# Kernel tuning notes

Hardware: AMD Instinct MI355X
Metric: run time of the kernel (lower is better)

Reference implementation:

```python
import jax, jax.numpy as jnp
import numpy as np

HIDDEN = 1024
N_HEADS = 16
HEAD = HIDDEN // N_HEADS
BATCH = 8
SEQ = 1024


def setup_inputs() -> dict:
    key = jax.random.key(0)
    ks = jax.random.split(key, 9)
    s = 0.02
    return {
        "x": jax.random.normal(ks[0], (BATCH, SEQ, HIDDEN), dtype=jnp.float32),
        "wq": jax.random.normal(ks[1], (HIDDEN, HIDDEN), dtype=jnp.float32) * s,
        "bq": jnp.zeros((HIDDEN,), dtype=jnp.float32),
        "wk": jax.random.normal(ks[2], (HIDDEN, HIDDEN), dtype=jnp.float32) * s,
        "bk": jnp.zeros((HIDDEN,), dtype=jnp.float32),
        "wv": jax.random.normal(ks[3], (HIDDEN, HIDDEN), dtype=jnp.float32) * s,
        "bv": jnp.zeros((HIDDEN,), dtype=jnp.float32),
        "wo": jax.random.normal(ks[4], (HIDDEN, HIDDEN), dtype=jnp.float32) * s,
        "bo": jnp.zeros((HIDDEN,), dtype=jnp.float32),
    }


def _split_heads(t):
    # [b, s, hidden] -> [b, head, s, head_size]
    b, s, _ = t.shape
    return t.reshape(b, s, N_HEADS, HEAD).transpose(0, 2, 1, 3)


def reference(x, wq, bq, wk, bk, wv, bv, wo, bo):
    # Linear layers (torch nn.Linear: y = x @ W.T + b); here weights stored as [in, out]
    q = _split_heads(x @ wq + bq)
    k = _split_heads(x @ wk + bk)
    v = _split_heads(x @ wv + bv)
    # NOTE: original scales by 1/sqrt(hidden_size), not 1/sqrt(head_size)
    scores = jnp.einsum("bhqd,bhkd->bhqk", q, k) / jnp.sqrt(jnp.float32(HIDDEN))
    attn = jax.nn.softmax(scores, axis=-1)
    combined = jnp.einsum("bhqk,bhkd->bhqd", attn, v)
    merged = combined.transpose(0, 2, 1, 3).reshape(x.shape[0], x.shape[1], HIDDEN)
    return merged @ wo + bo
```

## Files before the change

kernel.cpp:

```cpp
#include <hip/hip_runtime.h>
#include <hip/hip_bf16.h>

#define HIDDEN 1024
#define NHEADS 16
#define HEADD  64
#define BATCH  8
#define SEQ    1024
#define MROWS  (BATCH*SEQ)

typedef __bf16 bf16x8 __attribute__((ext_vector_type(8)));
typedef float  floatx4 __attribute__((ext_vector_type(4)));
typedef unsigned short ushort8_t __attribute__((ext_vector_type(8)));
typedef _Float16 f16x4 __attribute__((ext_vector_type(4)));
typedef _Float16 f16x2 __attribute__((ext_vector_type(2)));
typedef const __attribute__((address_space(1))) unsigned int* gas_u32p;
typedef __attribute__((address_space(3))) unsigned int* las_u32p;

__device__ __forceinline__ unsigned short f2bf(float f) {
  __hip_bfloat16 h = __float2bfloat16(f);
  return __builtin_bit_cast(unsigned short, h);
}

__device__ __forceinline__ bf16x8 ld_bf8(const unsigned short* p) {
  ushort8_t u = *(const ushort8_t*)p;
  return __builtin_bit_cast(bf16x8, u);
}

__device__ __forceinline__ f16x2 pk_f16(float a, float b) {
  return __builtin_bit_cast(f16x2, __builtin_amdgcn_cvt_pkrtz(a, b));
}

__device__ __forceinline__ void gload_lds16(const void* g, void* l) {
  __builtin_amdgcn_global_load_lds((gas_u32p)g, (las_u32p)l, 16, 0, 0);
}

__global__ __launch_bounds__(256) void cast_x_kernel(const float* __restrict__ in,
                                                     unsigned short* __restrict__ out) {
  int i = blockIdx.x * 256 + threadIdx.x;
  float4 v = ((const float4*)in)[i];
  ushort4 o = make_ushort4(f2bf(v.x), f2bf(v.y), f2bf(v.z), f2bf(v.w));
  ((ushort4*)out)[i] = o;
}

__global__ __launch_bounds__(256) void transpose_cast_w_kernel(
    const float* __restrict__ w0, const float* __restrict__ w1,
    const float* __restrict__ w2, const float* __restrict__ w3,
    unsigned short* __restrict__ o0, unsigned short* __restrict__ o1,
    unsigned short* __restrict__ o2, unsigned short* __restrict__ o3) {
  __shared__ __align__(16) unsigned short tile[64 * 68];
  const float* src = (blockIdx.z == 0) ? w0 : (blockIdx.z == 1) ? w1 : (blockIdx.z == 2) ? w2 : w3;
  unsigned short* dst = (blockIdx.z == 0) ? o0 : (blockIdx.z == 1) ? o1 : (blockIdx.z == 2) ? o2 : o3;
  const int k0 = blockIdx.x * 64, n0 = blockIdx.y * 64;
  const int tid = threadIdx.x;
#pragma unroll
  for (int it = 0; it < 4; ++it) {
    int c = tid + 256 * it;
    int row = c >> 4, f4 = c & 15;
    float4 v = *(const float4*)(src + (size_t)(k0 + row) * HIDDEN + n0 + 4 * f4);
    ushort4 u = make_ushort4(f2bf(v.x), f2bf(v.y), f2bf(v.z), f2bf(v.w));
    *(ushort4*)(&tile[row * 68 + 4 * f4]) = u;
  }
  __syncthreads();
#pragma unroll
  for (int it = 0; it < 2; ++it) {
    int c = tid + 256 * it;
    int nrow = c >> 3, kc = (c & 7) * 8;
    ushort8_t u;
#pragma unroll
    for (int j = 0; j < 8; ++j) u[j] = tile[(kc + j) * 68 + nrow];
    *(ushort8_t*)(dst + (size_t)(n0 + nrow) * HIDDEN + k0 + kc) = u;
  }
}

#define LDSA(buf, ks) ((buf) * 49152 + (ks) * 8192)
#define LDSB(buf, ks) ((buf) * 49152 + 16384 + (ks) * 16384)

#define BAR __builtin_amdgcn_s_barrier()
#define WLG do { asm volatile("s_waitcnt lgkmcnt(0)" ::: "memory"); \
                 __builtin_amdgcn_sched_barrier(0); } while (0)
#define WVM(n) asm volatile("s_waitcnt vmcnt(" #n ")" ::: "memory")

#define RDP(buf, ks) do {                                                          \
    _Pragma("unroll") for (int m_ = 0; m_ < 4; ++m_)                               \
      af[m_] = *(const bf16x8*)(ldsb + LDSA(buf, ks) +                             \
                                (wm * 64 + 16 * m_ + lr) * 64 + colx);             \
    _Pragma("unroll") for (int n_ = 0; n_ < 4; ++n_)                               \
      bc[n_] = *(const bf16x8*)(ldsb + LDSB(buf, ks) +                             \
                                (wn * 64 + 16 * n_ + lr) * 64 + colx);             \
  } while (0)

#define MM do {                                                                    \
    __builtin_amdgcn_s_setprio(1);                                                 \
    _Pragma("unroll") for (int m_ = 0; m_ < 4; ++m_)                               \
      _Pragma("unroll") for (int n_ = 0; n_ < 4; ++n_)                             \
        acc[m_][n_] = __builtin_amdgcn_mfma_f32_16x16x32_bf16(                     \
            af[m_], bc[n_], acc[m_][n_], 0, 0, 0);                                 \
    __builtin_amdgcn_s_setprio(0);                                                 \
  } while (0)

#define STG(buf, ks, kt) do {                                                      \
    int go_ = (kt) * 128 + (ks) * 64;                                              \
    gload_lds16(aS + go_,  ldsb + LDSA(buf, ks) + tid * 16);                       \
    gload_lds16(bS0 + go_, ldsb + LDSB(buf, ks) + tid * 16);                       \
    gload_lds16(bS1 + go_, ldsb + LDSB(buf, ks) + 8192 + tid * 16);                \
  } while (0)

template <int OUT>
__device__ __forceinline__ void gemm256_body(
    const unsigned short* __restrict__ A,
    const unsigned short* __restrict__ Bt,
    const float* __restrict__ bias,
    char* __restrict__ C, int ldC, float scale,
    char* ldsb) {
  const int tid = threadIdx.x;
  const int lane = tid & 63;
  const int wid = tid >> 6;
  const int wm = wid >> 2, wn = wid & 3;
  const int lr = lane & 15, q = lane >> 4;
  const int colx = (16 * q) ^ (((lr >> 3) & 1) << 5);

  const char *aS, *bS0, *bS1;
  {
    int linA = tid * 16;
    int lgA = linA ^ (((linA >> 9) & 1) << 5);
    aS = (const char*)A + (lgA >> 6) * 2048 + (lgA & 63);
    int linB0 = tid * 16, linB1 = 8192 + tid * 16;
    int lgB0 = linB0 ^ (((linB0 >> 9) & 1) << 5);
    int lgB1 = linB1 ^ (((linB1 >> 9) & 1) << 5);
    bS0 = (const char*)Bt + (lgB0 >> 6) * 2048 + (lgB0 & 63);
    bS1 = (const char*)Bt + (lgB1 >> 6) * 2048 + (lgB1 & 63);
  }

  floatx4 acc[4][4] = {};
  bf16x8 af[4], bc[4];

  STG(0, 0, 0); STG(0, 1, 0); STG(1, 0, 1);
  WVM(6);
  BAR;

  for (int i = 0; i < 7; ++i) {
    const int t1 = 2 * i + 1;
    RDP(0, 0); STG(1, 1, t1);     BAR; WVM(6); WLG; MM; BAR;
    RDP(0, 1); STG(0, 0, t1 + 1); BAR; WVM(6); WLG; MM; BAR;
    RDP(1, 0); STG(0, 1, t1 + 1); BAR; WVM(6); WLG; MM; BAR;
    RDP(1, 1); STG(1, 0, t1 + 2); BAR; WVM(6); WLG; MM; BAR;
  }
  RDP(0, 0); STG(1, 1, 15); BAR; WVM(6); WLG; MM; BAR;
  RDP(0, 1);                BAR; WVM(3); WLG; MM; BAR;
  RDP(1, 0);                BAR; WVM(0); WLG; MM; BAR;
  RDP(1, 1);                BAR;         WLG; MM;

  float cb[4];
  if constexpr (OUT != 2) {
#pragma unroll
    for (int n_ = 0; n_ < 4; ++n_) cb[n_] = bias[wn * 64 + 16 * n_ + lr];
  }
#pragma unroll
  for (int m_ = 0; m_ < 4; ++m_) {
    int row = wm * 64 + 16 * m_ + q * 4;
    float rb[4];
    if constexpr (OUT == 2) {
      float4 t = *(const float4*)&bias[row];
      rb[0] = t.x; rb[1] = t.y; rb[2] = t.z; rb[3] = t.w;
    }
#pragma unroll
    for (int n_ = 0; n_ < 4; ++n_) {
      int col = wn * 64 + 16 * n_ + lr;
#pragma unroll
      for (int r = 0; r < 4; ++r) {
        float v = (acc[m_][n_][r] + (OUT == 2 ? rb[r] : cb[n_])) * scale;
        int idx = (row + r) * ldC + col;
        if constexpr (OUT == 1)      ((unsigned short*)C)[idx] = f2bf(v);
        else if constexpr (OUT == 2) ((_Float16*)C)[idx] = (_Float16)v;
        else                         ((float*)C)[idx] = v;
      }
    }
  }
}

__global__ __launch_bounds__(512, 2) void gemm_qkv256_kernel(
    const unsigned short* __restrict__ xb,
    const unsigned short* __restrict__ wqkt,
    const unsigned short* __restrict__ wvt,
    const float* __restrict__ bq, const float* __restrict__ bk, const float* __restrict__ bv,
    unsigned short* __restrict__ Qb, unsigned short* __restrict__ Kb,
    _Float16* __restrict__ Vtout, float qscale) {
  __shared__ __align__(16) char lds[2 * 49152];
  const int bid = blockIdx.x;
  const int x = bid & 7;
  const int j = bid >> 3;
  if (j < 64) {
    int mt = x * 8 + (j & 7);
    int nq = j >> 3;
    int m0 = mt * 128, n0 = nq * 256;
    bool isQ = n0 < HIDDEN;
    int nc = isQ ? n0 : n0 - HIDDEN;
    unsigned short* C = (isQ ? Qb : Kb) + (size_t)m0 * HIDDEN + nc;
    gemm256_body<1>(xb + (size_t)m0 * HIDDEN, wqkt + (size_t)n0 * HIDDEN,
                    (isQ ? bq : bk) + nc, (char*)C, HIDDEN, isQ ? qscale : 1.0f, lds);
  } else {
    int j2 = j - 64;
    int m0 = x * 128;
    int n0 = j2 * 256;
    gemm256_body<2>(wvt + (size_t)m0 * HIDDEN, xb + (size_t)n0 * HIDDEN, bv + m0,
                    (char*)(Vtout + (size_t)m0 * MROWS + n0), MROWS, 1.0f, lds);
  }
}

__global__ __launch_bounds__(512, 2) void gemm_out256_kernel(
    const unsigned short* __restrict__ Mg, const unsigned short* __restrict__ wot,
    const float* __restrict__ bo, float* __restrict__ out) {
  __shared__ __align__(16) char lds[2 * 49152];
  const int bid = blockIdx.x;
  const int x = bid & 7;
  const int j = bid >> 3;
  int mt = x * 8 + (j & 7);
  int nt = j >> 3;
  int m0 = mt * 128, n0 = nt * 256;
  gemm256_body<0>(Mg + (size_t)m0 * HIDDEN, wot + (size_t)n0 * HIDDEN, bo + n0,
                  (char*)(out + (size_t)m0 * HIDDEN + n0), HIDDEN, 1.0f, lds);
}

#undef RDP
#undef MM
#undef STG
#undef BAR
#undef WLG
#undef WVM
#undef LDSA
#undef LDSB

__global__ __launch_bounds__(64, 2) void attn_kernel(
    const unsigned short* __restrict__ Qb,
    const unsigned short* __restrict__ Kb,
    const _Float16* __restrict__ Vtb,
    unsigned short* __restrict__ Og) {
  __shared__ __align__(16) unsigned short Ks[2][2][32 * 32];
  __shared__ __align__(16) _Float16      Vs[2][64 * 32];

  const int lane = threadIdx.x & 63;
  const int l = lane & 15, Q8 = lane >> 4;
  const int id = blockIdx.x;
  const int b = id & 7;
  const int h = (id >> 3) & 15;
  const int qt = id >> 7;
  const int q0 = qt * 64;

  const size_t qkbase = ((size_t)b * SEQ) * HIDDEN + (size_t)h * HEADD;

  bf16x8 bq[2][4];
#pragma unroll
  for (int nt = 0; nt < 4; ++nt) {
    const unsigned short* qr = Qb + qkbase + (size_t)(q0 + 16 * nt + l) * HIDDEN + Q8 * 8;
    bq[0][nt] = ld_bf8(qr);
    bq[1][nt] = ld_bf8(qr + 32);
  }

  const unsigned short* kg = Kb + qkbase;
  const _Float16* vg = Vtb + (size_t)(h * HEADD) * MROWS + (size_t)b * SEQ;
  const int r4 = lane >> 2;
  const int c4 = (lane & 3) * 8;

  auto stage = [&](int buf, int key0) {
#pragma unroll
    for (int p = 0; p < 2; ++p)
#pragma unroll
      for (int hl = 0; hl < 2; ++hl)
        gload_lds16(kg + (size_t)(key0 + 16 * hl + r4) * HIDDEN + 32 * p + c4,
                    &Ks[buf][p][(16 * hl) * 32]);
#pragma unroll
    for (int j = 0; j < 4; ++j)
      gload_lds16((const void*)(vg + (size_t)(16 * j + r4) * MROWS + key0 + c4),
                  (void*)&Vs[buf][(16 * j) * 32]);
  };

  floatx4 oacc[4][4] = {};
  float lsum[4] = {};

  stage(0, 0);

  for (int kt = 0; kt < SEQ / 32; ++kt) {
    const int cbuf = kt & 1;
    __syncthreads();
    if (kt + 1 < SEQ / 32) stage(cbuf ^ 1, (kt + 1) * 32);

#pragma unroll
    for (int g = 0; g < 2; ++g) {
      bf16x8 aK0 = ld_bf8(&Ks[cbuf][0][(16 * g + l) * 32 + Q8 * 8]);
      bf16x8 aK1 = ld_bf8(&Ks[cbuf][1][(16 * g + l) * 32 + Q8 * 8]);
      floatx4 sT[4] = {};
#pragma unroll
      for (int nt = 0; nt < 4; ++nt) {
        sT[nt] = __builtin_amdgcn_mfma_f32_16x16x32_bf16(aK0, bq[0][nt], sT[nt], 0, 0, 0);
        sT[nt] = __builtin_amdgcn_mfma_f32_16x16x32_bf16(aK1, bq[1][nt], sT[nt], 0, 0, 0);
      }

      f16x4 pf[4];
#pragma unroll
      for (int nt = 0; nt < 4; ++nt) {
        float p0 = __builtin_amdgcn_exp2f(sT[nt][0]);
        float p1 = __builtin_amdgcn_exp2f(sT[nt][1]);
        float p2 = __builtin_amdgcn_exp2f(sT[nt][2]);
        float p3 = __builtin_amdgcn_exp2f(sT[nt][3]);
        lsum[nt] += (p0 + p1) + (p2 + p3);
        f16x2 lo = pk_f16(p0, p1);
        f16x2 hi = pk_f16(p2, p3);
        pf[nt][0] = lo[0]; pf[nt][1] = lo[1]; pf[nt][2] = hi[0]; pf[nt][3] = hi[1];
      }

#pragma unroll
      for (int dt = 0; dt < 4; ++dt) {
        f16x4 vf = *(const f16x4*)&Vs[cbuf][(16 * dt + l) * 32 + 16 * g + 4 * Q8];
#pragma unroll
        for (int nt = 0; nt < 4; ++nt)
          oacc[dt][nt] = __builtin_amdgcn_mfma_f32_16x16x16f16(vf, pf[nt], oacc[dt][nt], 0, 0, 0);
      }
    }
  }

  float inv[4];
#pragma unroll
  for (int nt = 0; nt < 4; ++nt) {
    float s = lsum[nt];
    s += __shfl_xor(s, 16);
    s += __shfl_xor(s, 32);
    inv[nt] = 1.0f / s;
  }

#pragma unroll
  for (int nt = 0; nt < 4; ++nt) {
    unsigned short* orow = Og + qkbase + (size_t)(q0 + 16 * nt + l) * HIDDEN + 4 * Q8;
#pragma unroll
    for (int dt = 0; dt < 4; ++dt) {
      ushort4 o = make_ushort4(f2bf(oacc[dt][nt][0] * inv[nt]),
                               f2bf(oacc[dt][nt][1] * inv[nt]),
                               f2bf(oacc[dt][nt][2] * inv[nt]),
                               f2bf(oacc[dt][nt][3] * inv[nt]));
      *(ushort4*)(orow + 16 * dt) = o;
    }
  }
}

extern "C" void kernel_launch(void* const* d_in, const int* in_sizes, int n_in,
                              void* d_out, int out_size, void* d_ws, size_t ws_size,
                              hipStream_t stream) {
  const float* x  = (const float*)d_in[0];
  const float* wq = (const float*)d_in[1];
  const float* bq = (const float*)d_in[2];
  const float* wk = (const float*)d_in[3];
  const float* bk = (const float*)d_in[4];
  const float* wv = (const float*)d_in[5];
  const float* bv = (const float*)d_in[6];
  const float* wo = (const float*)d_in[7];
  const float* bo = (const float*)d_in[8];

  char* ws = (char*)d_ws;
  const size_t XB = (size_t)MROWS * HIDDEN * 2;
  const size_t WB = (size_t)HIDDEN * HIDDEN * 2;
  unsigned short* xb  = (unsigned short*)(ws);
  unsigned short* wqt = (unsigned short*)(ws + XB);
  unsigned short* wkt = (unsigned short*)(ws + XB + WB);
  unsigned short* wvt = (unsigned short*)(ws + XB + 2 * WB);
  unsigned short* wot = (unsigned short*)(ws + XB + 3 * WB);
  unsigned short* Qb  = (unsigned short*)(ws + XB + 4 * WB);
  unsigned short* Kb  = (unsigned short*)(ws + 2 * XB + 4 * WB);
  _Float16*       Vtb = (_Float16*)      (ws + 3 * XB + 4 * WB);
  unsigned short* Mg  = (unsigned short*)(ws + 4 * XB + 4 * WB);

  cast_x_kernel<<<(MROWS * HIDDEN / 4) / 256, 256, 0, stream>>>(x, xb);
  transpose_cast_w_kernel<<<dim3(16, 16, 4), 256, 0, stream>>>(wq, wk, wv, wo, wqt, wkt, wvt, wot);

  const float SQSCALE = 1.44269504088896f / 32.0f;
  gemm_qkv256_kernel<<<dim3(768), 512, 0, stream>>>(
      xb, wqt, wvt, bq, bk, bv, Qb, Kb, Vtb, SQSCALE);

  attn_kernel<<<dim3(SEQ / 64 * NHEADS * BATCH), 64, 0, stream>>>(Qb, Kb, Vtb, Mg);

  gemm_out256_kernel<<<dim3(256), 512, 0, stream>>>(Mg, wot, bo, (float*)d_out);
}
```

Measured before the change: 235.4 us.

## Use K=32 double-buffered pipeline in QKV GEMM to halve LDS and raise occupancy

The QKV projection GEMM now stages one 32-wide K slice per buffer (two buffers of 24 KB) instead of two 64-wide double-slice buffers (96 KB), and launch bounds go from 2 to 4 blocks per CU. The main loop becomes a simple two-stage ping-pong with a rolled loop. The output GEMM keeps the old deeper pipeline in its own body. The aim is higher occupancy to hide latency, at the cost of a shallower prefetch depth and more barriers per K step.

Result: slower. 240.6 us (+2.2%).

```diff
diff --git a/kernel.cpp b/kernel.cpp
--- a/kernel.cpp
+++ b/kernel.cpp
@@ -72,24 +72,24 @@
   }
 }
 
-#define LDSA(buf, ks) ((buf) * 49152 + (ks) * 8192)
-#define LDSB(buf, ks) ((buf) * 49152 + 16384 + (ks) * 16384)
-
 #define BAR __builtin_amdgcn_s_barrier()
 #define WLG do { asm volatile("s_waitcnt lgkmcnt(0)" ::: "memory"); \
                  __builtin_amdgcn_sched_barrier(0); } while (0)
 #define WVM(n) asm volatile("s_waitcnt vmcnt(" #n ")" ::: "memory")
 
-#define RDP(buf, ks) do {                                                          \
+#define LDSA2(buf) ((buf) * 24576)
+#define LDSB2(buf) ((buf) * 24576 + 8192)
+
+#define RDP2(buf) do {                                                             \
     _Pragma("unroll") for (int m_ = 0; m_ < 4; ++m_)                               \
-      af[m_] = *(const bf16x8*)(ldsb + LDSA(buf, ks) +                             \
+      af[m_] = *(const bf16x8*)(ldsb + LDSA2(buf) +                                \
                                 (wm * 64 + 16 * m_ + lr) * 64 + colx);             \
     _Pragma("unroll") for (int n_ = 0; n_ < 4; ++n_)                               \
-      bc[n_] = *(const bf16x8*)(ldsb + LDSB(buf, ks) +                             \
+      bc[n_] = *(const bf16x8*)(ldsb + LDSB2(buf) +                                \
                                 (wn * 64 + 16 * n_ + lr) * 64 + colx);             \
   } while (0)
 
-#define MM do {                                                                    \
+#define MM2 do {                                                                   \
     __builtin_amdgcn_s_setprio(1);                                                 \
     _Pragma("unroll") for (int m_ = 0; m_ < 4; ++m_)                               \
       _Pragma("unroll") for (int n_ = 0; n_ < 4; ++n_)                             \
@@ -98,15 +98,15 @@
     __builtin_amdgcn_s_setprio(0);                                                 \
   } while (0)
 
-#define STG(buf, ks, kt) do {                                                      \
-    int go_ = (kt) * 128 + (ks) * 64;                                              \
-    gload_lds16(aS + go_,  ldsb + LDSA(buf, ks) + tid * 16);                       \
-    gload_lds16(bS0 + go_, ldsb + LDSB(buf, ks) + tid * 16);                       \
-    gload_lds16(bS1 + go_, ldsb + LDSB(buf, ks) + 8192 + tid * 16);                \
+#define STG2(buf, t) do {                                                          \
+    int go_ = (t) * 64;                                                            \
+    gload_lds16(aS + go_,  ldsb + LDSA2(buf) + tid * 16);                          \
+    gload_lds16(bS0 + go_, ldsb + LDSB2(buf) + tid * 16);                          \
+    gload_lds16(bS1 + go_, ldsb + LDSB2(buf) + 8192 + tid * 16);                   \
   } while (0)
 
 template <int OUT>
-__device__ __forceinline__ void gemm256_body(
+__device__ __forceinline__ void gemm_qkv32_body(
     const unsigned short* __restrict__ A,
     const unsigned short* __restrict__ Bt,
     const float* __restrict__ bias,
@@ -134,21 +134,14 @@
   floatx4 acc[4][4] = {};
   bf16x8 af[4], bc[4];
 
-  STG(0, 0, 0); STG(0, 1, 0); STG(1, 0, 1);
-  WVM(6);
-  BAR;
-
-  for (int i = 0; i < 7; ++i) {
-    const int t1 = 2 * i + 1;
-    RDP(0, 0); STG(1, 1, t1);     BAR; WVM(6); WLG; MM; BAR;
-    RDP(0, 1); STG(0, 0, t1 + 1); BAR; WVM(6); WLG; MM; BAR;
-    RDP(1, 0); STG(0, 1, t1 + 1); BAR; WVM(6); WLG; MM; BAR;
-    RDP(1, 1); STG(1, 0, t1 + 2); BAR; WVM(6); WLG; MM; BAR;
-  }
-  RDP(0, 0); STG(1, 1, 15); BAR; WVM(6); WLG; MM; BAR;
-  RDP(0, 1);                BAR; WVM(3); WLG; MM; BAR;
-  RDP(1, 0);                BAR; WVM(0); WLG; MM; BAR;
-  RDP(1, 1);                BAR;         WLG; MM;
+  STG2(0, 0);
+#pragma unroll 1
+  for (int i = 0; i < 15; ++i) {
+    STG2(1, 2 * i + 1); WVM(3); BAR; RDP2(0); WLG; MM2; BAR;
+    STG2(0, 2 * i + 2); WVM(3); BAR; RDP2(1); WLG; MM2; BAR;
+  }
+  STG2(1, 31); WVM(3); BAR; RDP2(0); WLG; MM2; BAR;
+               WVM(0); BAR; RDP2(1); WLG; MM2;
 
   float cb[4];
   if constexpr (OUT != 2) {
@@ -170,22 +163,123 @@
       for (int r = 0; r < 4; ++r) {
         float v = (acc[m_][n_][r] + (OUT == 2 ? rb[r] : cb[n_])) * scale;
         int idx = (row + r) * ldC + col;
-        if constexpr (OUT == 1)      ((unsigned short*)C)[idx] = f2bf(v);
-        else if constexpr (OUT == 2) ((_Float16*)C)[idx] = (_Float16)v;
-        else                         ((float*)C)[idx] = v;
+        if constexpr (OUT == 1) ((unsigned short*)C)[idx] = f2bf(v);
+        else                    ((_Float16*)C)[idx] = (_Float16)v;
       }
     }
   }
 }
 
-__global__ __launch_bounds__(512, 2) void gemm_qkv256_kernel(
+#undef RDP2
+#undef MM2
+#undef STG2
+#undef LDSA2
+#undef LDSB2
+
+#define LDSA(buf, ks) ((buf) * 49152 + (ks) * 8192)
+#define LDSB(buf, ks) ((buf) * 49152 + 16384 + (ks) * 16384)
+
+#define RDP(buf, ks) do {                                                          \
+    _Pragma("unroll") for (int m_ = 0; m_ < 4; ++m_)                               \
+      af[m_] = *(const bf16x8*)(ldsb + LDSA(buf, ks) +                             \
+                                (wm * 64 + 16 * m_ + lr) * 64 + colx);             \
+    _Pragma("unroll") for (int n_ = 0; n_ < 4; ++n_)                               \
+      bc[n_] = *(const bf16x8*)(ldsb + LDSB(buf, ks) +                             \
+                                (wn * 64 + 16 * n_ + lr) * 64 + colx);             \
+  } while (0)
+
+#define MM do {                                                                    \
+    __builtin_amdgcn_s_setprio(1);                                                 \
+    _Pragma("unroll") for (int m_ = 0; m_ < 4; ++m_)                               \
+      _Pragma("unroll") for (int n_ = 0; n_ < 4; ++n_)                             \
+        acc[m_][n_] = __builtin_amdgcn_mfma_f32_16x16x32_bf16(                     \
+            af[m_], bc[n_], acc[m_][n_], 0, 0, 0);                                 \
+    __builtin_amdgcn_s_setprio(0);                                                 \
+  } while (0)
+
+#define STG(buf, ks, kt) do {                                                      \
+    int go_ = (kt) * 128 + (ks) * 64;                                              \
+    gload_lds16(aS + go_,  ldsb + LDSA(buf, ks) + tid * 16);                       \
+    gload_lds16(bS0 + go_, ldsb + LDSB(buf, ks) + tid * 16);                       \
+    gload_lds16(bS1 + go_, ldsb + LDSB(buf, ks) + 8192 + tid * 16);                \
+  } while (0)
+
+__device__ __forceinline__ void gemm_out_body(
+    const unsigned short* __restrict__ A, const unsigned short* __restrict__ Bt,
+    const float* __restrict__ bias, char* __restrict__ C, int ldC, char* ldsb) {
+  const int tid = threadIdx.x;
+  const int lane = tid & 63;
+  const int wid = tid >> 6;
+  const int wm = wid >> 2, wn = wid & 3;
+  const int lr = lane & 15, q = lane >> 4;
+  const int colx = (16 * q) ^ (((lr >> 3) & 1) << 5);
+
+  const char *aS, *bS0, *bS1;
+  {
+    int linA = tid * 16;
+    int lgA = linA ^ (((linA >> 9) & 1) << 5);
+    aS = (const char*)A + (lgA >> 6) * 2048 + (lgA & 63);
+    int linB0 = tid * 16, linB1 = 8192 + tid * 16;
+    int lgB0 = linB0 ^ (((linB0 >> 9) & 1) << 5);
+    int lgB1 = linB1 ^ (((linB1 >> 9) & 1) << 5);
+    bS0 = (const char*)Bt + (lgB0 >> 6) * 2048 + (lgB0 & 63);
+    bS1 = (const char*)Bt + (lgB1 >> 6) * 2048 + (lgB1 & 63);
+  }
+
+  floatx4 acc[4][4] = {};
+  bf16x8 af[4], bc[4];
+
+  STG(0, 0, 0); STG(0, 1, 0); STG(1, 0, 1);
+  WVM(6);
+  BAR;
+
+  for (int i = 0; i < 7; ++i) {
+    const int t1 = 2 * i + 1;
+    RDP(0, 0); STG(1, 1, t1);     BAR; WVM(6); WLG; MM; BAR;
+    RDP(0, 1); STG(0, 0, t1 + 1); BAR; WVM(6); WLG; MM; BAR;
+    RDP(1, 0); STG(0, 1, t1 + 1); BAR; WVM(6); WLG; MM; BAR;
+    RDP(1, 1); STG(1, 0, t1 + 2); BAR; WVM(6); WLG; MM; BAR;
+  }
+  RDP(0, 0); STG(1, 1, 15); BAR; WVM(6); WLG; MM; BAR;
+  RDP(0, 1);                BAR; WVM(3); WLG; MM; BAR;
+  RDP(1, 0);                BAR; WVM(0); WLG; MM; BAR;
+  RDP(1, 1);                BAR;         WLG; MM;
+
+  float cb[4];
+#pragma unroll
+  for (int n_ = 0; n_ < 4; ++n_) cb[n_] = bias[wn * 64 + 16 * n_ + lr];
+#pragma unroll
+  for (int m_ = 0; m_ < 4; ++m_) {
+    int row = wm * 64 + 16 * m_ + q * 4;
+#pragma unroll
+    for (int n_ = 0; n_ < 4; ++n_) {
+      int col = wn * 64 + 16 * n_ + lr;
+#pragma unroll
+      for (int r = 0; r < 4; ++r) {
+        float v = acc[m_][n_][r] + cb[n_];
+        ((float*)C)[(row + r) * ldC + col] = v;
+      }
+    }
+  }
+}
+
+#undef RDP
+#undef MM
+#undef STG
+#undef LDSA
+#undef LDSB
+#undef BAR
+#undef WLG
+#undef WVM
+
+__global__ __launch_bounds__(512, 4) void gemm_qkv256_kernel(
     const unsigned short* __restrict__ xb,
     const unsigned short* __restrict__ wqkt,
     const unsigned short* __restrict__ wvt,
     const float* __restrict__ bq, const float* __restrict__ bk, const float* __restrict__ bv,
     unsigned short* __restrict__ Qb, unsigned short* __restrict__ Kb,
     _Float16* __restrict__ Vtout, float qscale) {
-  __shared__ __align__(16) char lds[2 * 49152];
+  __shared__ __align__(16) char lds[2 * 24576];
   const int bid = blockIdx.x;
   const int x = bid & 7;
   const int j = bid >> 3;
@@ -196,14 +290,14 @@
     bool isQ = n0 < HIDDEN;
     int nc = isQ ? n0 : n0 - HIDDEN;
     unsigned short* C = (isQ ? Qb : Kb) + (size_t)m0 * HIDDEN + nc;
-    gemm256_body<1>(xb + (size_t)m0 * HIDDEN, wqkt + (size_t)n0 * HIDDEN,
-                    (isQ ? bq : bk) + nc, (char*)C, HIDDEN, isQ ? qscale : 1.0f, lds);
+    gemm_qkv32_body<1>(xb + (size_t)m0 * HIDDEN, wqkt + (size_t)n0 * HIDDEN,
+                       (isQ ? bq : bk) + nc, (char*)C, HIDDEN, isQ ? qscale : 1.0f, lds);
   } else {
     int j2 = j - 64;
     int m0 = x * 128;
     int n0 = j2 * 256;
-    gemm256_body<2>(wvt + (size_t)m0 * HIDDEN, xb + (size_t)n0 * HIDDEN, bv + m0,
-                    (char*)(Vtout + (size_t)m0 * MROWS + n0), MROWS, 1.0f, lds);
+    gemm_qkv32_body<2>(wvt + (size_t)m0 * HIDDEN, xb + (size_t)n0 * HIDDEN, bv + m0,
+                       (char*)(Vtout + (size_t)m0 * MROWS + n0), MROWS, 1.0f, lds);
   }
 }
 
@@ -217,18 +311,9 @@
   int mt = x * 8 + (j & 7);
   int nt = j >> 3;
   int m0 = mt * 128, n0 = nt * 256;
-  gemm256_body<0>(Mg + (size_t)m0 * HIDDEN, wot + (size_t)n0 * HIDDEN, bo + n0,
-                  (char*)(out + (size_t)m0 * HIDDEN + n0), HIDDEN, 1.0f, lds);
-}
-
-#undef RDP
-#undef MM
-#undef STG
-#undef BAR
-#undef WLG
-#undef WVM
-#undef LDSA
-#undef LDSB
+  gemm_out_body(Mg + (size_t)m0 * HIDDEN, wot + (size_t)n0 * HIDDEN, bo + n0,
+                (char*)(out + (size_t)m0 * HIDDEN + n0), HIDDEN, lds);
+}
 
 __global__ __launch_bounds__(64, 2) void attn_kernel(
     const unsigned short* __restrict__ Qb,
```

## Shrink GEMM K-step to 32 with double buffer for higher occupancy

Applied to the files above, without the earlier changes.

Replaces the 4-stage BK=64 pipelined GEMM body with a simpler double-buffered BK=32 loop that uses much less LDS. This allows more resident workgroups per CU (launch bounds raised to 6 and 4). The output projection also switches to 128x128 tiles with twice as many blocks. The trade-off is more barriers per K-step and less prefetch depth, in exchange for latency hiding through occupancy.

Measured after the change: 611.5 us. 2.6x slower.

```diff
diff --git a/kernel.cpp b/kernel.cpp
--- a/kernel.cpp
+++ b/kernel.cpp
@@ -72,46 +72,29 @@
   }
 }
 
-#define LDSA(buf, ks) ((buf) * 49152 + (ks) * 8192)
-#define LDSB(buf, ks) ((buf) * 49152 + 16384 + (ks) * 16384)
-
 #define BAR __builtin_amdgcn_s_barrier()
 #define WLG do { asm volatile("s_waitcnt lgkmcnt(0)" ::: "memory"); \
                  __builtin_amdgcn_sched_barrier(0); } while (0)
-#define WVM(n) asm volatile("s_waitcnt vmcnt(" #n ")" ::: "memory")
-
-#define RDP(buf, ks) do {                                                          \
-    _Pragma("unroll") for (int m_ = 0; m_ < 4; ++m_)                               \
-      af[m_] = *(const bf16x8*)(ldsb + LDSA(buf, ks) +                             \
-                                (wm * 64 + 16 * m_ + lr) * 64 + colx);             \
-    _Pragma("unroll") for (int n_ = 0; n_ < 4; ++n_)                               \
-      bc[n_] = *(const bf16x8*)(ldsb + LDSB(buf, ks) +                             \
-                                (wn * 64 + 16 * n_ + lr) * 64 + colx);             \
-  } while (0)
-
-#define MM do {                                                                    \
-    __builtin_amdgcn_s_setprio(1);                                                 \
-    _Pragma("unroll") for (int m_ = 0; m_ < 4; ++m_)                               \
-      _Pragma("unroll") for (int n_ = 0; n_ < 4; ++n_)                             \
-        acc[m_][n_] = __builtin_amdgcn_mfma_f32_16x16x32_bf16(                     \
-            af[m_], bc[n_], acc[m_][n_], 0, 0, 0);                                 \
-    __builtin_amdgcn_s_setprio(0);                                                 \
-  } while (0)
-
-#define STG(buf, ks, kt) do {                                                      \
-    int go_ = (kt) * 128 + (ks) * 64;                                              \
-    gload_lds16(aS + go_,  ldsb + LDSA(buf, ks) + tid * 16);                       \
-    gload_lds16(bS0 + go_, ldsb + LDSB(buf, ks) + tid * 16);                       \
-    gload_lds16(bS1 + go_, ldsb + LDSB(buf, ks) + 8192 + tid * 16);                \
-  } while (0)
-
-template <int OUT>
-__device__ __forceinline__ void gemm256_body(
+
+template <int N> __device__ __forceinline__ void wvm() {
+  if constexpr (N == 0)      asm volatile("s_waitcnt vmcnt(0)" ::: "memory");
+  else if constexpr (N == 2) asm volatile("s_waitcnt vmcnt(2)" ::: "memory");
+  else if constexpr (N == 3) asm volatile("s_waitcnt vmcnt(3)" ::: "memory");
+}
+
+template <int OUT, int BN>
+__device__ __forceinline__ void gemm_bk32_body(
     const unsigned short* __restrict__ A,
     const unsigned short* __restrict__ Bt,
     const float* __restrict__ bias,
     char* __restrict__ C, int ldC, float scale,
     char* ldsb) {
+  constexpr int NF = BN / 64;
+  constexpr int WNC = BN / 4;
+  constexpr int BUFST = 8192 + BN * 64;
+  constexpr int NB2 = (BN == 256);
+  constexpr int VC = NB2 ? 3 : 2;
+
   const int tid = threadIdx.x;
   const int lane = tid & 63;
   const int wid = tid >> 6;
@@ -131,29 +114,48 @@
     bS1 = (const char*)Bt + (lgB1 >> 6) * 2048 + (lgB1 & 63);
   }
 
-  floatx4 acc[4][4] = {};
-  bf16x8 af[4], bc[4];
-
-  STG(0, 0, 0); STG(0, 1, 0); STG(1, 0, 1);
-  WVM(6);
-  BAR;
-
-  for (int i = 0; i < 7; ++i) {
-    const int t1 = 2 * i + 1;
-    RDP(0, 0); STG(1, 1, t1);     BAR; WVM(6); WLG; MM; BAR;
-    RDP(0, 1); STG(0, 0, t1 + 1); BAR; WVM(6); WLG; MM; BAR;
-    RDP(1, 0); STG(0, 1, t1 + 1); BAR; WVM(6); WLG; MM; BAR;
-    RDP(1, 1); STG(1, 0, t1 + 2); BAR; WVM(6); WLG; MM; BAR;
-  }
-  RDP(0, 0); STG(1, 1, 15); BAR; WVM(6); WLG; MM; BAR;
-  RDP(0, 1);                BAR; WVM(3); WLG; MM; BAR;
-  RDP(1, 0);                BAR; WVM(0); WLG; MM; BAR;
-  RDP(1, 1);                BAR;         WLG; MM;
-
-  float cb[4];
+  floatx4 acc[4][NF] = {};
+  bf16x8 af[4], bc[NF];
+
+  auto stg = [&](int buf, int t) {
+    int go = t * 64;
+    char* base = ldsb + buf * BUFST;
+    gload_lds16(aS + go,  base + tid * 16);
+    gload_lds16(bS0 + go, base + 8192 + tid * 16);
+    if constexpr (NB2) gload_lds16(bS1 + go, base + 16384 + tid * 16);
+  };
+  auto rdp = [&](int buf) {
+    char* base = ldsb + buf * BUFST;
+#pragma unroll
+    for (int m_ = 0; m_ < 4; ++m_)
+      af[m_] = *(const bf16x8*)(base + (wm * 64 + 16 * m_ + lr) * 64 + colx);
+#pragma unroll
+    for (int n_ = 0; n_ < NF; ++n_)
+      bc[n_] = *(const bf16x8*)(base + 8192 + (wn * WNC + 16 * n_ + lr) * 64 + colx);
+  };
+  auto mm = [&]() {
+    __builtin_amdgcn_s_setprio(1);
+#pragma unroll
+    for (int m_ = 0; m_ < 4; ++m_)
+#pragma unroll
+      for (int n_ = 0; n_ < NF; ++n_)
+        acc[m_][n_] = __builtin_amdgcn_mfma_f32_16x16x32_bf16(af[m_], bc[n_], acc[m_][n_], 0, 0, 0);
+    __builtin_amdgcn_s_setprio(0);
+  };
+
+  stg(0, 0);
+#pragma unroll 1
+  for (int i = 0; i < 15; ++i) {
+    stg(1, 2 * i + 1); wvm<VC>(); BAR; rdp(0); WLG; mm(); BAR;
+    stg(0, 2 * i + 2); wvm<VC>(); BAR; rdp(1); WLG; mm(); BAR;
+  }
+  stg(1, 31); wvm<VC>(); BAR; rdp(0); WLG; mm(); BAR;
+              wvm<0>();  BAR; rdp(1); WLG; mm();
+
+  float cb[NF];
   if constexpr (OUT != 2) {
 #pragma unroll
-    for (int n_ = 0; n_ < 4; ++n_) cb[n_] = bias[wn * 64 + 16 * n_ + lr];
+    for (int n_ = 0; n_ < NF; ++n_) cb[n_] = bias[wn * WNC + 16 * n_ + lr];
   }
 #pragma unroll
   for (int m_ = 0; m_ < 4; ++m_) {
@@ -164,8 +166,8 @@
       rb[0] = t.x; rb[1] = t.y; rb[2] = t.z; rb[3] = t.w;
     }
 #pragma unroll
-    for (int n_ = 0; n_ < 4; ++n_) {
-      int col = wn * 64 + 16 * n_ + lr;
+    for (int n_ = 0; n_ < NF; ++n_) {
+      int col = wn * WNC + 16 * n_ + lr;
 #pragma unroll
       for (int r = 0; r < 4; ++r) {
         float v = (acc[m_][n_][r] + (OUT == 2 ? rb[r] : cb[n_])) * scale;
@@ -178,14 +180,14 @@
   }
 }
 
-__global__ __launch_bounds__(512, 2) void gemm_qkv256_kernel(
+__global__ __launch_bounds__(512, 6) void gemm_qkv256_kernel(
     const unsigned short* __restrict__ xb,
     const unsigned short* __restrict__ wqkt,
     const unsigned short* __restrict__ wvt,
     const float* __restrict__ bq, const float* __restrict__ bk, const float* __restrict__ bv,
     unsigned short* __restrict__ Qb, unsigned short* __restrict__ Kb,
     _Float16* __restrict__ Vtout, float qscale) {
-  __shared__ __align__(16) char lds[2 * 49152];
+  __shared__ __align__(16) char lds[2 * (8192 + 16384)];
   const int bid = blockIdx.x;
   const int x = bid & 7;
   const int j = bid >> 3;
@@ -196,39 +198,33 @@
     bool isQ = n0 < HIDDEN;
     int nc = isQ ? n0 : n0 - HIDDEN;
     unsigned short* C = (isQ ? Qb : Kb) + (size_t)m0 * HIDDEN + nc;
-    gemm256_body<1>(xb + (size_t)m0 * HIDDEN, wqkt + (size_t)n0 * HIDDEN,
-                    (isQ ? bq : bk) + nc, (char*)C, HIDDEN, isQ ? qscale : 1.0f, lds);
+    gemm_bk32_body<1, 256>(xb + (size_t)m0 * HIDDEN, wqkt + (size_t)n0 * HIDDEN,
+                           (isQ ? bq : bk) + nc, (char*)C, HIDDEN, isQ ? qscale : 1.0f, lds);
   } else {
     int j2 = j - 64;
     int m0 = x * 128;
     int n0 = j2 * 256;
-    gemm256_body<2>(wvt + (size_t)m0 * HIDDEN, xb + (size_t)n0 * HIDDEN, bv + m0,
-                    (char*)(Vtout + (size_t)m0 * MROWS + n0), MROWS, 1.0f, lds);
-  }
-}
-
-__global__ __launch_bounds__(512, 2) void gemm_out256_kernel(
+    gemm_bk32_body<2, 256>(wvt + (size_t)m0 * HIDDEN, xb + (size_t)n0 * HIDDEN, bv + m0,
+                           (char*)(Vtout + (size_t)m0 * MROWS + n0), MROWS, 1.0f, lds);
+  }
+}
+
+__global__ __launch_bounds__(512, 4) void gemm_out256_kernel(
     const unsigned short* __restrict__ Mg, const unsigned short* __restrict__ wot,
     const float* __restrict__ bo, float* __restrict__ out) {
-  __shared__ __align__(16) char lds[2 * 49152];
+  __shared__ __align__(16) char lds[2 * (8192 + 8192)];
   const int bid = blockIdx.x;
   const int x = bid & 7;
   const int j = bid >> 3;
   int mt = x * 8 + (j & 7);
   int nt = j >> 3;
-  int m0 = mt * 128, n0 = nt * 256;
-  gemm256_body<0>(Mg + (size_t)m0 * HIDDEN, wot + (size_t)n0 * HIDDEN, bo + n0,
-                  (char*)(out + (size_t)m0 * HIDDEN + n0), HIDDEN, 1.0f, lds);
-}
-
-#undef RDP
-#undef MM
-#undef STG
+  int m0 = mt * 128, n0 = nt * 128;
+  gemm_bk32_body<0, 128>(Mg + (size_t)m0 * HIDDEN, wot + (size_t)n0 * HIDDEN, bo + n0,
+                         (char*)(out + (size_t)m0 * HIDDEN + n0), HIDDEN, 1.0f, lds);
+}
+
 #undef BAR
 #undef WLG
-#undef WVM
-#undef LDSA
-#undef LDSB
 
 __global__ __launch_bounds__(64, 2) void attn_kernel(
     const unsigned short* __restrict__ Qb,
@@ -376,5 +372,5 @@
 
   attn_kernel<<<dim3(SEQ / 64 * NHEADS * BATCH), 64, 0, stream>>>(Qb, Kb, Vtb, Mg);
 
-  gemm_out256_kernel<<<dim3(256), 512, 0, stream>>>(Mg, wot, bo, (float*)d_out);
-}
+  gemm_out256_kernel<<<dim3(512), 512, 0, stream>>>(Mg, wot, bo, (float*)d_out);
+}
```
